# Kernel optimization log

Measured on AMD Instinct MI355X. Metric: run time of the kernel, lower is better.

## Reference

```python
import jax, jax.numpy as jnp
import numpy as np

B, S, N1, D = 1, 2048, 16, 128   # batch, seq, attn heads, head dim
H, DI, K = 8, 128, 512           # indexer heads, indexer dim, top-k
SCALE = 1.0 / float(np.sqrt(D))
EPS = 1e-9


def setup_inputs() -> dict:
    key0 = jax.random.key(0)
    ks = jax.random.split(key0, 6)
    query = jax.random.normal(ks[0], (B, S, N1, D), jnp.float32)
    key = jax.random.normal(ks[1], (B, S, 1, D), jnp.float32)
    query_indexer = jax.random.normal(ks[2], (B, S, H, DI), jnp.float32)
    key_indexer = jax.random.normal(ks[3], (B, S, 1, DI), jnp.float32)
    weights = jax.random.normal(ks[4], (B, S, H), jnp.float32)
    # causal top-k indices: sorted random key positions clamped to <= t
    idx = jnp.sort(jax.random.randint(ks[5], (B, S, K), 0, S), axis=-1)
    sparse_indices = jnp.minimum(idx, jnp.arange(S)[None, :, None]).astype(jnp.int32)
    # flash-attention softmax stats of the causal attention, reused by the op
    scores = SCALE * jnp.einsum('btnd,bsd->bnts', query, key[:, :, 0, :])
    causal = jnp.arange(S)[:, None] >= jnp.arange(S)[None, :]
    masked = jnp.where(causal[None, None], scores, -1e30)
    softmax_max = masked.max(axis=-1)                              # [B,N1,S]
    softmax_sum = jnp.exp(masked - softmax_max[..., None]).sum(-1) # [B,N1,S]
    return {
        'query': query, 'key': key,
        'query_indexer': query_indexer, 'key_indexer': key_indexer,
        'weights': weights, 'sparse_indices': sparse_indices,
        'softmax_max': softmax_max, 'softmax_sum': softmax_sum,
    }


def reference(query, key, query_indexer, key_indexer, weights,
              sparse_indices, softmax_max, softmax_sum):
    # --- target: true attention distribution from reused softmax stats ---
    scores = SCALE * jnp.einsum('btnd,bsd->bnts', query, key[:, :, 0, :])  # [B,N1,S,S]
    causal = jnp.arange(S)[:, None] >= jnp.arange(S)[None, :]
    p = jnp.where(causal[None, None],
                  jnp.exp(scores - softmax_max[..., None]) / softmax_sum[..., None],
                  0.0)
    t_full = p.sum(axis=1)                                          # [B,S,S] head-summed
    p_sel = jnp.take_along_axis(t_full, sparse_indices, axis=2)     # [B,S,K]
    p_norm = p_sel / (p_sel.sum(axis=-1, keepdims=True) + EPS)
    # --- lightning indexer scores: sum_h w_h * relu(q_idx_h . k_idx) ---
    sim = jnp.einsum('bthd,bsd->bths', query_indexer, key_indexer[:, :, 0, :])  # [B,S,H,S]
    I_full = jnp.einsum('bth,bths->bts', weights, jax.nn.relu(sim))             # [B,S,S]
    I_sel = jnp.take_along_axis(I_full, sparse_indices, axis=2)                 # [B,S,K]
    logq = jax.nn.log_softmax(I_sel, axis=-1)
    # --- KL(target || indexer) over selected set, normalized by seq len ---
    kl = jnp.sum(p_norm * (jnp.log(p_norm + EPS) - logq))
    return kl / S
```

## Files before the change

### kernel.cpp

```cpp
#include <hip/hip_runtime.h>
#include <hip/hip_bf16.h>
#include <math.h>

#define S_LEN 2048
#define N1 16
#define D 128
#define H 8
#define DI 128
#define K_SEL 512
#define SCALE_F 0.08838834764831845f
#define EPS_F 1e-9f

typedef __attribute__((ext_vector_type(8))) __bf16 bf16x8;
typedef __attribute__((ext_vector_type(4))) float f32x4;
typedef unsigned char uchar;
typedef unsigned long long ulong64;

static __device__ __forceinline__ uint cvtpk_fp8(float a, float b) {
  uint r;
  asm volatile("v_cvt_pk_fp8_f32 %0, %1, %2" : "=v"(r) : "v"(a), "v"(b));
  return r & 0xffffu;
}
static __device__ __forceinline__ uint pack4_fp8(float4 v) {
  return cvtpk_fp8(v.x, v.y) | (cvtpk_fp8(v.z, v.w) << 16);
}

static __device__ __forceinline__ ushort f2bf(float x) {
  uint u = __float_as_uint(x);
  uint r = u + 0x7fffu + ((u >> 16) & 1u);
  return (ushort)(r >> 16);
}
static __device__ __forceinline__ bf16x8 cvt8(float4 v0, float4 v1) {
  bf16x8 a;
  a[0] = (__bf16)v0.x; a[1] = (__bf16)v0.y; a[2] = (__bf16)v0.z; a[3] = (__bf16)v0.w;
  a[4] = (__bf16)v1.x; a[5] = (__bf16)v1.y; a[6] = (__bf16)v1.z; a[7] = (__bf16)v1.w;
  return a;
}

__global__ __launch_bounds__(256)
void prep_comb8(const float* __restrict__ key, const float* __restrict__ kidx,
                uchar* __restrict__ comb) {
  const int gid = blockIdx.x * 256 + threadIdx.x;
  const int row = gid >> 5;
  const int i = gid & 31;
  *(uint*)(comb + (size_t)row * 256 + i * 4) = pack4_fp8(((const float4*)key)[gid]);
  *(uint*)(comb + (size_t)row * 256 + 128 + i * 4) = pack4_fp8(((const float4*)kidx)[gid]);
}

__global__ __launch_bounds__(256)
void prep_apack8(const float* __restrict__ query, const float* __restrict__ qidx,
                 uchar* __restrict__ ap, uchar* __restrict__ aip) {
  const int t = blockIdx.x * 4 + (threadIdx.x >> 6);
  const int lane = threadIdx.x & 63;
  const int lg = lane >> 4;
  const int lr = lane & 15;
#pragma unroll
  for (int ks = 0; ks < 4; ++ks) {
    const int off = ks * 32 + lg * 8;
    const float* s = query + (size_t)t * (N1 * D) + lr * D + off;
    const float4 v0 = *(const float4*)s;
    const float4 v1 = *(const float4*)(s + 4);
    const ulong64 u = (ulong64)pack4_fp8(v0) | ((ulong64)pack4_fp8(v1) << 32);
    *(ulong64*)(ap + ((size_t)(t * 4 + ks) * 64 + lane) * 8) = u;
    ulong64 ui = 0;
    if (lr < H) {
      const float* s2 = qidx + (size_t)t * (H * DI) + lr * DI + off;
      const float4 w0 = *(const float4*)s2;
      const float4 w1 = *(const float4*)(s2 + 4);
      ui = (ulong64)pack4_fp8(w0) | ((ulong64)pack4_fp8(w1) << 32);
    }
    *(ulong64*)(aip + ((size_t)(t * 4 + ks) * 64 + lane) * 8) = ui;
  }
}

#define STAGE8(TB, SVG)                                                        \
  do {                                                                         \
    _Pragma("unroll") for (int j_ = 0; j_ < 4; ++j_) {                         \
      const int r_ = 4 * j_ + (lane >> 4);                                     \
      const int srow_ = __shfl((SVG), r_);                                     \
      const uchar* src_ = comb + (size_t)srow_ * 256 +                         \
                          (((lane & 15) ^ (r_ & 15)) << 4);                    \
      __builtin_amdgcn_global_load_lds(                                        \
          (const __attribute__((address_space(1))) void*)(src_),               \
          (__attribute__((address_space(3))) void*)((TB) + j_ * 1024), 16, 0, 0);\
    }                                                                          \
  } while (0)

__global__ __launch_bounds__(256, 2)
void sli_kl_mfma8(const float* __restrict__ weights,
                  const int* __restrict__ sidx,
                  const float* __restrict__ smax,
                  const float* __restrict__ ssum,
                  const uchar* __restrict__ comb,
                  const uchar* __restrict__ apack,
                  const uchar* __restrict__ aipack,
                  float* __restrict__ pkl,
                  float* __restrict__ out) {
  const int t = blockIdx.x;
  const int tid = threadIdx.x;
  const int lane = tid & 63;
  const int w = tid >> 6;
  const int lg = lane >> 4;
  const int lr = lane & 15;

  __shared__ __align__(16) uchar tiles[4][2][4096];
  __shared__ float red[5][4];
  uchar* tb0 = &tiles[w][0][0];
  uchar* tb1 = &tiles[w][1][0];

  int sv[8];
#pragma unroll
  for (int g = 0; g < 8; ++g)
    sv[g] = sidx[t * K_SEL + w * 128 + g * 16 + lr];

  long aq[4], ai[4];
#pragma unroll
  for (int ks = 0; ks < 4; ++ks) {
    aq[ks] = *(const long*)(apack + ((size_t)(t * 4 + ks) * 64 + lane) * 8);
    ai[ks] = *(const long*)(aipack + ((size_t)(t * 4 + ks) * 64 + lane) * 8);
  }

  float cnl[4], wgl[4];
#pragma unroll
  for (int j = 0; j < 4; ++j) {
    const int head = lg * 4 + j;
    cnl[j] = __expf(-smax[head * S_LEN + t]) / ssum[head * S_LEN + t];
    wgl[j] = (head < H) ? weights[t * H + head] : 0.f;
  }

  __builtin_amdgcn_sched_barrier(0);
  STAGE8(tb0, sv[0]);
  STAGE8(tb1, sv[1]);
  __builtin_amdgcn_sched_barrier(0);

  float pa[8], ia[8];
#pragma unroll
  for (int g = 0; g < 8; ++g) {
    uchar* tb = (g & 1) ? tb1 : tb0;
    if (g < 7) {
      asm volatile("s_waitcnt vmcnt(4)" ::: "memory");
    } else {
      asm volatile("s_waitcnt vmcnt(0)" ::: "memory");
    }
    __builtin_amdgcn_sched_barrier(0);
    long bA[4], bI[4];
#pragma unroll
    for (int ks = 0; ks < 4; ++ks) {
      const int cgA = 2 * ks + (lg >> 1);
      const int cgI = 8 + 2 * ks + (lg >> 1);
      const int sub = (lg & 1) * 8;
      bA[ks] = *(const long*)(tb + lr * 256 + ((cgA ^ lr) << 4) + sub);
      bI[ks] = *(const long*)(tb + lr * 256 + ((cgI ^ lr) << 4) + sub);
    }
    __builtin_amdgcn_sched_barrier(0);
    asm volatile("s_waitcnt lgkmcnt(0)" ::: "memory");
    __builtin_amdgcn_sched_barrier(0);
    if (g < 6) STAGE8(tb, sv[g + 2]);
    f32x4 cA = {0.f, 0.f, 0.f, 0.f};
    f32x4 cI = {0.f, 0.f, 0.f, 0.f};
#pragma unroll
    for (int ks = 0; ks < 4; ++ks) {
      cA = __builtin_amdgcn_mfma_f32_16x16x32_fp8_fp8(aq[ks], bA[ks], cA, 0, 0, 0);
      cI = __builtin_amdgcn_mfma_f32_16x16x32_fp8_fp8(ai[ks], bI[ks], cI, 0, 0, 0);
    }
    float p = 0.f, e = 0.f;
#pragma unroll
    for (int j = 0; j < 4; ++j) {
      p = fmaf(__expf(cA[j] * SCALE_F), cnl[j], p);
      e = fmaf(wgl[j], fmaxf(cI[j], 0.f), e);
    }
    pa[g] = p;
    ia[g] = e;
  }

#pragma unroll
  for (int g = 0; g < 8; ++g) {
    pa[g] += __shfl_xor(pa[g], 16); pa[g] += __shfl_xor(pa[g], 32);
    ia[g] += __shfl_xor(ia[g], 16); ia[g] += __shfl_xor(ia[g], 32);
  }

  float la = 0.f, le = -INFINITY;
#pragma unroll
  for (int g = 0; g < 8; ++g) {
    la += pa[g];
    le = fmaxf(le, ia[g]);
  }
#pragma unroll
  for (int off = 8; off >= 1; off >>= 1) {
    la += __shfl_xor(la, off);
    le = fmaxf(le, __shfl_xor(le, off));
  }
  if (lane == 0) { red[0][w] = la; red[1][w] = le; }
  __syncthreads();
  const float S_a = red[0][0] + red[0][1] + red[0][2] + red[0][3];
  const float M = fmaxf(fmaxf(red[1][0], red[1][1]), fmaxf(red[1][2], red[1][3]));
  const float inv_sa = 1.f / (S_a + EPS_F);

  float z = 0.f, t1 = 0.f, t2 = 0.f;
#pragma unroll
  for (int g = 0; g < 8; ++g) {
    const float e = ia[g];
    const float pn = pa[g] * inv_sa;
    z += __expf(e - M);
    t1 += pn * __logf(pn + EPS_F);
    t2 += pn * e;
  }
#pragma unroll
  for (int off = 8; off >= 1; off >>= 1) {
    z += __shfl_xor(z, off);
    t1 += __shfl_xor(t1, off);
    t2 += __shfl_xor(t2, off);
  }
  if (lane == 0) { red[2][w] = z; red[3][w] = t1; red[4][w] = t2; }
  __syncthreads();

  if (tid == 0) {
    const float Z = red[2][0] + red[2][1] + red[2][2] + red[2][3];
    const float T1 = red[3][0] + red[3][1] + red[3][2] + red[3][3];
    const float T2 = red[4][0] + red[4][1] + red[4][2] + red[4][3];
    const float total_pn = S_a * inv_sa;
    const float kl_row = (T1 - T2 + (M + __logf(Z)) * total_pn) * (1.0f / (float)S_LEN);
    if (pkl) pkl[t] = kl_row;
    else atomicAdd(out, kl_row);
  }
}

__global__ __launch_bounds__(256)
void reduce_kl(const float* __restrict__ pkl, float* __restrict__ out) {
  const int tid = threadIdx.x;
  float s = 0.f;
  for (int i = tid; i < S_LEN; i += 256) s += pkl[i];
#pragma unroll
  for (int off = 32; off >= 1; off >>= 1) s += __shfl_xor(s, off);
  __shared__ float r[4];
  if ((tid & 63) == 0) r[tid >> 6] = s;
  __syncthreads();
  if (tid == 0) out[0] = r[0] + r[1] + r[2] + r[3];
}

__global__ __launch_bounds__(256)
void prep_comb(const float* __restrict__ key, const float* __restrict__ kidx,
               ushort* __restrict__ comb) {
  const int gid = blockIdx.x * 256 + threadIdx.x;
  const int row = gid >> 5;
  const int i = gid & 31;
  const float4 kv = ((const float4*)key)[gid];
  ushort4 o;
  o.x = f2bf(kv.x); o.y = f2bf(kv.y); o.z = f2bf(kv.z); o.w = f2bf(kv.w);
  *(ushort4*)(comb + (size_t)row * 256 + i * 4) = o;
  const float4 iv = ((const float4*)kidx)[gid];
  ushort4 p;
  p.x = f2bf(iv.x); p.y = f2bf(iv.y); p.z = f2bf(iv.z); p.w = f2bf(iv.w);
  *(ushort4*)(comb + (size_t)row * 256 + 128 + i * 4) = p;
}

__global__ __launch_bounds__(256)
void sli_kl_fused(const float* __restrict__ query,
                  const float* __restrict__ qidx,
                  const float* __restrict__ weights,
                  const int* __restrict__ sidx,
                  const float* __restrict__ smax,
                  const float* __restrict__ ssum,
                  const ushort* __restrict__ comb,
                  float* __restrict__ out) {
  const int t = blockIdx.x;
  const int tid = threadIdx.x;
  const int lane = tid & 63;
  const int w = tid >> 6;
  const int lg = lane >> 4;
  const int lr = lane & 15;
  __shared__ float red[5][4];

  int sv[8];
#pragma unroll
  for (int g = 0; g < 8; ++g)
    sv[g] = sidx[t * K_SEL + w * 128 + g * 16 + lr];

  bf16x8 aq[4], ai[4];
  {
    const float* qb = query + (size_t)t * (N1 * D) + lr * D;
#pragma unroll
    for (int ks = 0; ks < 4; ++ks) {
      const int off = ks * 32 + lg * 8;
      aq[ks] = cvt8(*(const float4*)(qb + off), *(const float4*)(qb + off + 4));
    }
    if (lr < H) {
      const float* ib = qidx + (size_t)t * (H * DI) + lr * DI;
#pragma unroll
      for (int ks = 0; ks < 4; ++ks) {
        const int off = ks * 32 + lg * 8;
        ai[ks] = cvt8(*(const float4*)(ib + off), *(const float4*)(ib + off + 4));
      }
    } else {
#pragma unroll
      for (int ks = 0; ks < 4; ++ks) {
        bf16x8 zz = {};
        ai[ks] = zz;
      }
    }
  }
  float cnl[4], wgl[4];
#pragma unroll
  for (int j = 0; j < 4; ++j) {
    const int head = lg * 4 + j;
    cnl[j] = __expf(-smax[head * S_LEN + t]) / ssum[head * S_LEN + t];
    wgl[j] = (head < H) ? weights[t * H + head] : 0.f;
  }
  float pa[8], ia[8];
#pragma unroll
  for (int g = 0; g < 8; ++g) {
    const ushort* rb = comb + (size_t)sv[g] * 256;
    f32x4 cA = {0.f, 0.f, 0.f, 0.f};
    f32x4 cI = {0.f, 0.f, 0.f, 0.f};
#pragma unroll
    for (int ks = 0; ks < 4; ++ks) {
      const bf16x8 vA = *(const bf16x8*)(rb + ks * 32 + lg * 8);
      const bf16x8 vI = *(const bf16x8*)(rb + 128 + ks * 32 + lg * 8);
      cA = __builtin_amdgcn_mfma_f32_16x16x32_bf16(aq[ks], vA, cA, 0, 0, 0);
      cI = __builtin_amdgcn_mfma_f32_16x16x32_bf16(ai[ks], vI, cI, 0, 0, 0);
    }
    float pp = 0.f, e = 0.f;
#pragma unroll
    for (int j = 0; j < 4; ++j) {
      pp = fmaf(__expf(cA[j] * SCALE_F), cnl[j], pp);
      e = fmaf(wgl[j], fmaxf(cI[j], 0.f), e);
    }
    pp += __shfl_xor(pp, 16); pp += __shfl_xor(pp, 32);
    e += __shfl_xor(e, 16); e += __shfl_xor(e, 32);
    pa[g] = pp;
    ia[g] = e;
  }
  float la = 0.f, le = -INFINITY;
#pragma unroll
  for (int g = 0; g < 8; ++g) { la += pa[g]; le = fmaxf(le, ia[g]); }
#pragma unroll
  for (int off = 8; off >= 1; off >>= 1) {
    la += __shfl_xor(la, off);
    le = fmaxf(le, __shfl_xor(le, off));
  }
  if (lane == 0) { red[0][w] = la; red[1][w] = le; }
  __syncthreads();
  const float S_a = red[0][0] + red[0][1] + red[0][2] + red[0][3];
  const float M = fmaxf(fmaxf(red[1][0], red[1][1]), fmaxf(red[1][2], red[1][3]));
  const float inv_sa = 1.f / (S_a + EPS_F);
  float z = 0.f, t1 = 0.f, t2 = 0.f;
#pragma unroll
  for (int g = 0; g < 8; ++g) {
    const float e = ia[g];
    const float pn = pa[g] * inv_sa;
    z += __expf(e - M);
    t1 += pn * __logf(pn + EPS_F);
    t2 += pn * e;
  }
#pragma unroll
  for (int off = 8; off >= 1; off >>= 1) {
    z += __shfl_xor(z, off);
    t1 += __shfl_xor(t1, off);
    t2 += __shfl_xor(t2, off);
  }
  if (lane == 0) { red[2][w] = z; red[3][w] = t1; red[4][w] = t2; }
  __syncthreads();
  if (tid == 0) {
    const float Z = red[2][0] + red[2][1] + red[2][2] + red[2][3];
    const float T1 = red[3][0] + red[3][1] + red[3][2] + red[3][3];
    const float T2 = red[4][0] + red[4][1] + red[4][2] + red[4][3];
    const float total_pn = S_a * inv_sa;
    atomicAdd(out, (T1 - T2 + (M + __logf(Z)) * total_pn) * (1.0f / (float)S_LEN));
  }
}

extern "C" void kernel_launch(void* const* d_in, const int* in_sizes, int n_in,
                              void* d_out, int out_size, void* d_ws, size_t ws_size,
                              hipStream_t stream) {
  const float* query = (const float*)d_in[0];
  const float* key = (const float*)d_in[1];
  const float* qidx = (const float*)d_in[2];
  const float* kidx = (const float*)d_in[3];
  const float* weights = (const float*)d_in[4];
  const int* sidx = (const int*)d_in[5];
  const float* smax = (const float*)d_in[6];
  const float* ssum = (const float*)d_in[7];
  float* out = (float*)d_out;

  const size_t apack_b = (size_t)S_LEN * 4 * 64 * 8;
  const size_t comb8_b = (size_t)S_LEN * 256;
  const size_t pkl_b = (size_t)S_LEN * sizeof(float);
  const size_t need = 2 * apack_b + comb8_b + pkl_b;

  if (ws_size >= need) {
    uchar* apack = (uchar*)d_ws;
    uchar* aipack = apack + apack_b;
    uchar* comb8 = aipack + apack_b;
    float* pkl = (float*)(comb8 + comb8_b);

    prep_comb8<<<dim3((S_LEN * D / 4) / 256), dim3(256), 0, stream>>>(key, kidx, comb8);
    prep_apack8<<<dim3(S_LEN / 4), dim3(256), 0, stream>>>(query, qidx, apack, aipack);
    sli_kl_mfma8<<<dim3(S_LEN), dim3(256), 0, stream>>>(
        weights, sidx, smax, ssum, comb8, apack, aipack, pkl, out);
    reduce_kl<<<dim3(1), dim3(256), 0, stream>>>(pkl, out);
  } else {
    ushort* comb = (ushort*)d_ws;
    hipMemsetAsync(out, 0, sizeof(float), stream);
    prep_comb<<<dim3((S_LEN * D / 4) / 256), dim3(256), 0, stream>>>(key, kidx, comb);
    sli_kl_fused<<<dim3(S_LEN), dim3(256), 0, stream>>>(
        query, qidx, weights, sidx, smax, ssum, comb, out);
  }
}
```

Before: 42.09 us.

## Merge prep kernels, replace final reduce with atomics, raise occupancy bound

The two FP8 packing kernels become one launch that splits work by block index, and the separate reduction kernel is replaced by a per-block atomicAdd into a memset-zeroed output. The main kernel's launch bounds go from 2 to 4 blocks per CU. This cuts launch count and per-launch overhead, which matters at this microsecond scale. The costs are 2048 contended atomics on a single address, a nondeterministic summation order, and possible register spilling under the tighter occupancy bound.

```diff
diff --git a/kernel.cpp b/kernel.cpp
--- a/kernel.cpp
+++ b/kernel.cpp
@@ -38,38 +38,40 @@
 }
 
 __global__ __launch_bounds__(256)
-void prep_comb8(const float* __restrict__ key, const float* __restrict__ kidx,
-                uchar* __restrict__ comb) {
-  const int gid = blockIdx.x * 256 + threadIdx.x;
-  const int row = gid >> 5;
-  const int i = gid & 31;
-  *(uint*)(comb + (size_t)row * 256 + i * 4) = pack4_fp8(((const float4*)key)[gid]);
-  *(uint*)(comb + (size_t)row * 256 + 128 + i * 4) = pack4_fp8(((const float4*)kidx)[gid]);
-}
-
-__global__ __launch_bounds__(256)
-void prep_apack8(const float* __restrict__ query, const float* __restrict__ qidx,
-                 uchar* __restrict__ ap, uchar* __restrict__ aip) {
-  const int t = blockIdx.x * 4 + (threadIdx.x >> 6);
-  const int lane = threadIdx.x & 63;
-  const int lg = lane >> 4;
-  const int lr = lane & 15;
-#pragma unroll
-  for (int ks = 0; ks < 4; ++ks) {
-    const int off = ks * 32 + lg * 8;
-    const float* s = query + (size_t)t * (N1 * D) + lr * D + off;
-    const float4 v0 = *(const float4*)s;
-    const float4 v1 = *(const float4*)(s + 4);
-    const ulong64 u = (ulong64)pack4_fp8(v0) | ((ulong64)pack4_fp8(v1) << 32);
-    *(ulong64*)(ap + ((size_t)(t * 4 + ks) * 64 + lane) * 8) = u;
-    ulong64 ui = 0;
-    if (lr < H) {
-      const float* s2 = qidx + (size_t)t * (H * DI) + lr * DI + off;
-      const float4 w0 = *(const float4*)s2;
-      const float4 w1 = *(const float4*)(s2 + 4);
-      ui = (ulong64)pack4_fp8(w0) | ((ulong64)pack4_fp8(w1) << 32);
-    }
-    *(ulong64*)(aip + ((size_t)(t * 4 + ks) * 64 + lane) * 8) = ui;
+void prep_all8(const float* __restrict__ key, const float* __restrict__ kidx,
+               const float* __restrict__ query, const float* __restrict__ qidx,
+               uchar* __restrict__ comb, uchar* __restrict__ ap,
+               uchar* __restrict__ aip) {
+  const int b = blockIdx.x;
+  if (b < 256) {
+    const int gid = b * 256 + threadIdx.x;
+    const int row = gid >> 5;
+    const int i = gid & 31;
+    *(uint*)(comb + (size_t)row * 256 + i * 4) = pack4_fp8(((const float4*)key)[gid]);
+    *(uint*)(comb + (size_t)row * 256 + 128 + i * 4) =
+        pack4_fp8(((const float4*)kidx)[gid]);
+  } else {
+    const int t = (b - 256) * 4 + (threadIdx.x >> 6);
+    const int lane = threadIdx.x & 63;
+    const int lg = lane >> 4;
+    const int lr = lane & 15;
+#pragma unroll
+    for (int ks = 0; ks < 4; ++ks) {
+      const int off = ks * 32 + lg * 8;
+      const float* s = query + (size_t)t * (N1 * D) + lr * D + off;
+      const float4 v0 = *(const float4*)s;
+      const float4 v1 = *(const float4*)(s + 4);
+      const ulong64 u = (ulong64)pack4_fp8(v0) | ((ulong64)pack4_fp8(v1) << 32);
+      *(ulong64*)(ap + ((size_t)(t * 4 + ks) * 64 + lane) * 8) = u;
+      ulong64 ui = 0;
+      if (lr < H) {
+        const float* s2 = qidx + (size_t)t * (H * DI) + lr * DI + off;
+        const float4 w0 = *(const float4*)s2;
+        const float4 w1 = *(const float4*)(s2 + 4);
+        ui = (ulong64)pack4_fp8(w0) | ((ulong64)pack4_fp8(w1) << 32);
+      }
+      *(ulong64*)(aip + ((size_t)(t * 4 + ks) * 64 + lane) * 8) = ui;
+    }
   }
 }
 
@@ -86,7 +88,7 @@
     }                                                                          \
   } while (0)
 
-__global__ __launch_bounds__(256, 2)
+__global__ __launch_bounds__(256, 4)
 void sli_kl_mfma8(const float* __restrict__ weights,
                   const int* __restrict__ sidx,
                   const float* __restrict__ smax,
@@ -94,7 +96,6 @@
                   const uchar* __restrict__ comb,
                   const uchar* __restrict__ apack,
                   const uchar* __restrict__ aipack,
-                  float* __restrict__ pkl,
                   float* __restrict__ out) {
   const int t = blockIdx.x;
   const int tid = threadIdx.x;
@@ -219,23 +220,8 @@
     const float T1 = red[3][0] + red[3][1] + red[3][2] + red[3][3];
     const float T2 = red[4][0] + red[4][1] + red[4][2] + red[4][3];
     const float total_pn = S_a * inv_sa;
-    const float kl_row = (T1 - T2 + (M + __logf(Z)) * total_pn) * (1.0f / (float)S_LEN);
-    if (pkl) pkl[t] = kl_row;
-    else atomicAdd(out, kl_row);
-  }
-}
-
-__global__ __launch_bounds__(256)
-void reduce_kl(const float* __restrict__ pkl, float* __restrict__ out) {
-  const int tid = threadIdx.x;
-  float s = 0.f;
-  for (int i = tid; i < S_LEN; i += 256) s += pkl[i];
-#pragma unroll
-  for (int off = 32; off >= 1; off >>= 1) s += __shfl_xor(s, off);
-  __shared__ float r[4];
-  if ((tid & 63) == 0) r[tid >> 6] = s;
-  __syncthreads();
-  if (tid == 0) out[0] = r[0] + r[1] + r[2] + r[3];
+    atomicAdd(out, (T1 - T2 + (M + __logf(Z)) * total_pn) * (1.0f / (float)S_LEN));
+  }
 }
 
 __global__ __launch_bounds__(256)
@@ -384,23 +370,21 @@
 
   const size_t apack_b = (size_t)S_LEN * 4 * 64 * 8;
   const size_t comb8_b = (size_t)S_LEN * 256;
-  const size_t pkl_b = (size_t)S_LEN * sizeof(float);
-  const size_t need = 2 * apack_b + comb8_b + pkl_b;
+  const size_t need = 2 * apack_b + comb8_b;
+
+  hipMemsetAsync(out, 0, sizeof(float), stream);
 
   if (ws_size >= need) {
     uchar* apack = (uchar*)d_ws;
     uchar* aipack = apack + apack_b;
     uchar* comb8 = aipack + apack_b;
-    float* pkl = (float*)(comb8 + comb8_b);
-
-    prep_comb8<<<dim3((S_LEN * D / 4) / 256), dim3(256), 0, stream>>>(key, kidx, comb8);
-    prep_apack8<<<dim3(S_LEN / 4), dim3(256), 0, stream>>>(query, qidx, apack, aipack);
+
+    prep_all8<<<dim3(256 + S_LEN / 4), dim3(256), 0, stream>>>(
+        key, kidx, query, qidx, comb8, apack, aipack);
     sli_kl_mfma8<<<dim3(S_LEN), dim3(256), 0, stream>>>(
-        weights, sidx, smax, ssum, comb8, apack, aipack, pkl, out);
-    reduce_kl<<<dim3(1), dim3(256), 0, stream>>>(pkl, out);
+        weights, sidx, smax, ssum, comb8, apack, aipack, out);
   } else {
     ushort* comb = (ushort*)d_ws;
-    hipMemsetAsync(out, 0, sizeof(float), stream);
     prep_comb<<<dim3((S_LEN * D / 4) / 256), dim3(256), 0, stream>>>(key, kidx, comb);
     sli_kl_fused<<<dim3(S_LEN), dim3(256), 0, stream>>>(
         query, qidx, weights, sidx, smax, ssum, comb, out);
```

Result: slower. 53.90 us (+28.1%).
